# Optimization experiments

Measured on AMD Instinct MI355X. Metric: run time of the kernel, lower is better.

## Reference

```python
import jax, jax.numpy as jnp
import numpy as np

N = 500_000
K = 16
E = N * K
H = 256


def _linear_params(key, fan_in, fan_out):
    k1, k2 = jax.random.split(key)
    bound = 1.0 / np.sqrt(fan_in)
    W = jax.random.uniform(k1, (fan_in, fan_out), jnp.float32, -bound, bound)
    b = jax.random.uniform(k2, (fan_out,), jnp.float32, -bound, bound)
    return W, b


def setup_inputs() -> dict:
    key = jax.random.key(0)
    ks = jax.random.split(key, 10)
    x = jax.random.normal(ks[0], (N, 3), jnp.float32)
    edge_index = jax.random.randint(ks[1], (2, E), 0, N, jnp.int64)
    edge_attr = jax.random.normal(ks[2], (E, 1), jnp.float32)
    W1, b1 = _linear_params(ks[3], K, H)          # GNN1 message MLP: Linear(k, 256)
    We1, be1 = _linear_params(ks[4], H, 128)      # encoder Linear(256,128)
    We2, be2 = _linear_params(ks[5], 128, 6)      # encoder Linear(128,6)
    Wd1, bd1 = _linear_params(ks[6], 6, 128)      # decoder Linear(6,128)
    Wd2, bd2 = _linear_params(ks[7], 128, H)      # decoder Linear(128,256)
    Wo, bo = _linear_params(ks[8], H, 1)          # output Linear(256,1)
    return {"x": x, "edge_index": edge_index, "edge_attr": edge_attr,
            "W1": W1, "b1": b1, "We1": We1, "be1": be1, "We2": We2, "be2": be2,
            "Wd1": Wd1, "bd1": bd1, "Wd2": Wd2, "bd2": bd2, "Wo": Wo, "bo": bo}


def reference(x, edge_index, edge_attr, W1, b1, We1, be1, We2, be2,
              Wd1, bd1, Wd2, bd2, Wo, bo):
    # GNN1: messages are edge_attr verbatim (x_i/x_j ignored); aggregate reshapes
    # all E scalar messages into (N, k) (k edges per node, contiguous) and runs
    # Linear(k,256)+Tanh. Note: LSTM and GCN4 branches in the torch code are dead
    # (GNN1 ignores its node-feature input), so they do not affect the output.
    k = W1.shape[0]
    msgs = edge_attr.reshape(-1, k)                    # (N, k)
    h = jnp.tanh(msgs @ W1 + b1)                       # (N, 256)
    # second L1 call produces the identical result (depends only on edge_attr)
    z = jnp.tanh(jnp.tanh(h @ We1 + be1) @ We2 + be2)  # encoder -> (N, 6)
    d = jnp.tanh(z @ Wd1 + bd1) @ Wd2 + bd2            # decoder -> (N, 256)
    out = jax.nn.sigmoid(jnp.tanh(d) @ Wo + bo)        # (N, 1)
    return out[:, 0]                                   # squeeze(dim=1) -> (N,)
```

## Files before the change

kernel.cpp:

```cpp
#include <hip/hip_runtime.h>


#define N_NODES 500000

#define OFF_W1 0
#define OFF_W2 8192
#define OFF_W3 73728
#define OFF_W4 77824
#define OFF_W5 86016
#define OFF_WO 151552
#define OFF_B1 152576
#define OFF_B2 153600
#define OFF_B3 154112
#define OFF_B4 154176
#define OFF_B5 154688
#define OFF_EXTRA 155712
#define OFF_ZERO  155728
#define IMG_END   156240
#define IMG_ALLOC 156672

#define K1_B1    77824
#define K1_B2    78848
#define K1_B3    79360
#define K1_Z     79872
#define K1_LDS   80384
#define K2_LDS   76800
#define K2_W4    0
#define K2_W5    8192
#define K2_WO    73728
#define K2_B4    74752
#define K2_B5    75264

#define SCONST (-2.8853900817779268f)

typedef _Float16 half8  __attribute__((ext_vector_type(8)));
typedef __fp16   pk16x2 __attribute__((ext_vector_type(2)));
typedef float    f32x4  __attribute__((ext_vector_type(4)));
typedef int      int4v  __attribute__((ext_vector_type(4)));

__device__ __align__(16) char g_img[IMG_ALLOC];

static __device__ __forceinline__ unsigned pack_f16_rne(float a, float b) {
  _Float16 ha = (_Float16)a, hb = (_Float16)b;
  unsigned short ua = __builtin_bit_cast(unsigned short, ha);
  unsigned short ub = __builtin_bit_cast(unsigned short, hb);
  return (unsigned)ua | ((unsigned)ub << 16);
}
static __device__ __forceinline__ int pkrtz(float a, float b) {
  pk16x2 h = __builtin_amdgcn_cvt_pkrtz(a, b);
  return __builtin_bit_cast(int, h);
}
static __device__ __forceinline__ float sig2(float y) {
  float e = __builtin_amdgcn_exp2f(y);
  return __builtin_amdgcn_rcpf(1.0f + e);
}
static __device__ __forceinline__ float sigmoid_f(float x) {
  float e = __builtin_amdgcn_exp2f(x * -1.4426950408889634f);
  return __builtin_amdgcn_rcpf(1.0f + e);
}
static __device__ __forceinline__ f32x4 mfma16(half8 a, int4v b, f32x4 c) {
  return __builtin_amdgcn_mfma_f32_16x16x32_f16(a, __builtin_bit_cast(half8, b), c, 0, 0, 0);
}
static __device__ __forceinline__ half8 lda(const char* smem, int off) {
  return *(const half8*)(smem + off);
}
static __device__ __forceinline__ f32x4 ldf4(const char* smem, int off) {
  return *(const f32x4*)(smem + off);
}
#define FENCE() __builtin_amdgcn_sched_barrier(0)

struct PK2 { int lo, hi; };
static __device__ __forceinline__ PK2 tp(f32x4 a) {
  PK2 p;
  p.lo = pkrtz(sig2(a.x), sig2(a.y));
  p.hi = pkrtz(sig2(a.z), sig2(a.w));
  return p;
}

__global__ void gnn_prep(const float* __restrict__ W1,  const float* __restrict__ b1,
                         const float* __restrict__ We1, const float* __restrict__ be1,
                         const float* __restrict__ We2, const float* __restrict__ be2,
                         const float* __restrict__ Wd1, const float* __restrict__ bd1,
                         const float* __restrict__ Wd2, const float* __restrict__ bd2,
                         const float* __restrict__ Wo,  const float* __restrict__ bo)
{
  int t = blockIdx.x * 256 + threadIdx.x;
  int off = t * 4;
  if (off >= IMG_END) return;
  unsigned val;
  if (off < OFF_W2) {
    int rel = off;
    int mi = rel >> 9, li = (rel >> 4) & 31, j2 = (rel >> 2) & 3;
    int fout = mi * 16 + (li & 15);
    int k0 = (li >> 4) * 8 + j2 * 2;
    val = pack_f16_rne(SCONST * W1[k0 * 256 + fout], SCONST * W1[(k0 + 1) * 256 + fout]);
  } else if (off < OFF_W3) {
    int rel = off - OFF_W2;
    int blk = rel >> 10, li = (rel >> 4) & 63, j2 = (rel >> 2) & 3;
    int mi = blk >> 3, ki = blk & 7;
    int fout = mi * 16 + (li & 15);
    int k0 = ki * 32 + 4 * (li >> 4) + 16 * (j2 >> 1) + 2 * (j2 & 1);
    val = pack_f16_rne(2.0f * SCONST * We1[k0 * 128 + fout],
                       2.0f * SCONST * We1[(k0 + 1) * 128 + fout]);
  } else if (off < OFF_W4) {
    int rel = off - OFF_W3;
    int ki = rel >> 10, li = (rel >> 4) & 63, j2 = (rel >> 2) & 3;
    int fo = li & 15;
    int k0 = ki * 32 + 4 * (li >> 4) + 16 * (j2 >> 1) + 2 * (j2 & 1);
    float a = (fo < 6) ? 2.0f * SCONST * We2[k0 * 6 + fo] : 0.0f;
    float b = (fo < 6) ? 2.0f * SCONST * We2[(k0 + 1) * 6 + fo] : 0.0f;
    val = pack_f16_rne(a, b);
  } else if (off < OFF_W5) {
    int rel = off - OFF_W4;
    int mi = rel >> 10, li = (rel >> 4) & 63, j2 = (rel >> 2) & 3;
    int fout = mi * 16 + (li & 15);
    int qa = li >> 4;
    unsigned v = 0;
    if (j2 < 2) {
      int k0 = 4 * qa + 2 * j2;
      float a = (k0 < 6)     ? 2.0f * SCONST * Wd1[k0 * 128 + fout]       : 0.0f;
      float b = (k0 + 1 < 6) ? 2.0f * SCONST * Wd1[(k0 + 1) * 128 + fout] : 0.0f;
      v = pack_f16_rne(a, b);
    }
    val = v;
  } else if (off < OFF_WO) {
    int rel = off - OFF_W5;
    int blk = rel >> 10, li = (rel >> 4) & 63, j2 = (rel >> 2) & 3;
    int mi = blk >> 2, ki = blk & 3;
    int fout = mi * 16 + (li & 15);
    int k0 = ki * 32 + 4 * (li >> 4) + 16 * (j2 >> 1) + 2 * (j2 & 1);
    val = pack_f16_rne(2.0f * SCONST * Wd2[k0 * 256 + fout],
                       2.0f * SCONST * Wd2[(k0 + 1) * 256 + fout]);
  } else if (off < OFF_B1) {
    val = __builtin_bit_cast(unsigned, 2.0f * Wo[(off - OFF_WO) >> 2]);
  } else if (off < OFF_B2) {
    val = __builtin_bit_cast(unsigned, SCONST * b1[(off - OFF_B1) >> 2]);
  } else if (off < OFF_B3) {
    int i = (off - OFF_B2) >> 2;
    float s = 0.0f;
    for (int k = 0; k < 256; ++k) s += We1[k * 128 + i];
    val = __builtin_bit_cast(unsigned, SCONST * (be1[i] - s));
  } else if (off < OFF_B4) {
    int i = (off - OFF_B3) >> 2;
    float v = 0.0f;
    if (i < 6) {
      float s = 0.0f;
      for (int k = 0; k < 128; ++k) s += We2[k * 6 + i];
      v = SCONST * (be2[i] - s);
    }
    val = __builtin_bit_cast(unsigned, v);
  } else if (off < OFF_B5) {
    int i = (off - OFF_B4) >> 2;
    float s = 0.0f;
    for (int k = 0; k < 6; ++k) s += Wd1[k * 128 + i];
    val = __builtin_bit_cast(unsigned, SCONST * (bd1[i] - s));
  } else if (off < OFF_EXTRA) {
    int i = (off - OFF_B5) >> 2;
    float s = 0.0f;
    for (int k = 0; k < 128; ++k) s += Wd2[k * 256 + i];
    val = __builtin_bit_cast(unsigned, SCONST * (bd2[i] - s));
  } else if (off == OFF_EXTRA) {
    float s = 0.0f;
    for (int k = 0; k < 256; ++k) s += Wo[k];
    val = __builtin_bit_cast(unsigned, bo[0] - s);
  } else {
    val = 0;
  }
  *(unsigned*)(g_img + off) = val;
}

static __device__ __forceinline__ void stage_chunk(const char* src, char* dst) {
  __builtin_amdgcn_global_load_lds(
      (const __attribute__((address_space(1))) void*)src,
      (__attribute__((address_space(3))) void*)dst, 16, 0, 0);
}

#define L1_PAIR(KO, OUT_G0, OUT_G1) do {                                   \
    half8 Ae = lda(smem, w1b + (2*(KO))*w1s);                              \
    half8 Ao = lda(smem, w1b + (2*(KO)+1)*w1s);                            \
    f32x4 be_ = ldf4(smem, K1_B1 + (2*(KO))*64 + q*16);                    \
    f32x4 bo_ = ldf4(smem, K1_B1 + (2*(KO)+1)*64 + q*16);                  \
    f32x4 ae0 = mfma16(Ae, b1g0, be_);                                     \
    f32x4 ae1 = mfma16(Ae, b1g1, be_);                                     \
    f32x4 ao0 = mfma16(Ao, b1g0, bo_);                                     \
    f32x4 ao1 = mfma16(Ao, b1g1, bo_);                                     \
    PK2 pe0 = tp(ae0), po0 = tp(ao0), pe1 = tp(ae1), po1 = tp(ao1);        \
    OUT_G0.x = pe0.lo; OUT_G0.y = pe0.hi; OUT_G0.z = po0.lo; OUT_G0.w = po0.hi; \
    OUT_G1.x = pe1.lo; OUT_G1.y = pe1.hi; OUT_G1.z = po1.lo; OUT_G1.w = po1.hi; \
    FENCE();                                                               \
  } while (0)

#define L2_MI(MI, ACC0, ACC1) do {                                                            \
    f32x4 bb = ldf4(smem, K1_B2 + (MI)*64 + q*16);                                            \
    ACC0 = bb; ACC1 = bb;                                                                     \
    half8 A;                                                                                  \
    A = lda(smem, OFF_W2 + ((MI)*8+0)*1024 + ln*16); ACC0 = mfma16(A, c2g0_0, ACC0); ACC1 = mfma16(A, c2g1_0, ACC1); \
    A = lda(smem, OFF_W2 + ((MI)*8+1)*1024 + ln*16); ACC0 = mfma16(A, c2g0_1, ACC0); ACC1 = mfma16(A, c2g1_1, ACC1); \
    A = lda(smem, OFF_W2 + ((MI)*8+2)*1024 + ln*16); ACC0 = mfma16(A, c2g0_2, ACC0); ACC1 = mfma16(A, c2g1_2, ACC1); \
    A = lda(smem, OFF_W2 + ((MI)*8+3)*1024 + ln*16); ACC0 = mfma16(A, c2g0_3, ACC0); ACC1 = mfma16(A, c2g1_3, ACC1); \
    A = lda(smem, OFF_W2 + ((MI)*8+4)*1024 + ln*16); ACC0 = mfma16(A, c2g0_4, ACC0); ACC1 = mfma16(A, c2g1_4, ACC1); \
    A = lda(smem, OFF_W2 + ((MI)*8+5)*1024 + ln*16); ACC0 = mfma16(A, c2g0_5, ACC0); ACC1 = mfma16(A, c2g1_5, ACC1); \
    A = lda(smem, OFF_W2 + ((MI)*8+6)*1024 + ln*16); ACC0 = mfma16(A, c2g0_6, ACC0); ACC1 = mfma16(A, c2g1_6, ACC1); \
    A = lda(smem, OFF_W2 + ((MI)*8+7)*1024 + ln*16); ACC0 = mfma16(A, c2g0_7, ACC0); ACC1 = mfma16(A, c2g1_7, ACC1); \
  } while (0)

#define L2_PAIR(KO, OUT_G0, OUT_G1) do {                                   \
    f32x4 ve0, ve1, vo0, vo1;                                              \
    L2_MI(2*(KO),   ve0, ve1);                                             \
    FENCE();                                                               \
    L2_MI(2*(KO)+1, vo0, vo1);                                             \
    PK2 pe0 = tp(ve0), po0 = tp(vo0), pe1 = tp(ve1), po1 = tp(vo1);        \
    OUT_G0.x = pe0.lo; OUT_G0.y = pe0.hi; OUT_G0.z = po0.lo; OUT_G0.w = po0.hi; \
    OUT_G1.x = pe1.lo; OUT_G1.y = pe1.hi; OUT_G1.z = po1.lo; OUT_G1.w = po1.hi; \
    FENCE();                                                               \
  } while (0)

__global__ __launch_bounds__(512)
void gnn_k1(const float* __restrict__ ea, int4v* __restrict__ zbuf)
{
  __shared__ __align__(16) char smem[K1_LDS];
  const int tid = threadIdx.x;
  const int wv = tid >> 6, ln = tid & 63;

#pragma unroll 1
  for (int r = 0; r < 10; ++r) {
    int cb = (r * 8 + wv) << 6;
    if (cb < 5024) {
      int src;
      if (cb < 4864)      src = cb * 16;
      else if (cb < 4992) src = OFF_B1 + (cb - 4864) * 16;
      else                src = OFF_ZERO + (cb - 4992) * 16;
      stage_chunk(g_img + src + ln * 16, smem + (size_t)cb * 16 + ln * 16);
    }
  }
  __syncthreads();

  const int q = ln >> 4, c = ln & 15;
  const bool qlo = (q < 2);
  const int lnl16 = (ln & 31) * 16;
  const int w1b = qlo ? (OFF_W1 + lnl16) : (K1_Z + lnl16);
  const int w1s = qlo ? 512 : 0;

  const int NT = (N_NODES + 255) / 256;
#pragma unroll 1
  for (int t = blockIdx.x; t < NT; t += gridDim.x) {
    const int base = t * 256 + wv * 32;

    int nl = base + (q >> 1) * 16 + c;
    if (nl > N_NODES - 1) nl = N_NODES - 1;
    const f32x4* ea4 = (const f32x4*)ea;
    size_t eb = (size_t)nl * 4 + (size_t)((q & 1) * 2);
    f32x4 vlo = ea4[eb];
    f32x4 vhi = ea4[eb + 1];
    int4v b1g0;
    b1g0.x = pkrtz(vlo.x, vlo.y); b1g0.y = pkrtz(vlo.z, vlo.w);
    b1g0.z = pkrtz(vhi.x, vhi.y); b1g0.w = pkrtz(vhi.z, vhi.w);
    int sh = (ln + 32) & 63;
    int4v b1g1;
    b1g1.x = __shfl(b1g0.x, sh, 64); b1g1.y = __shfl(b1g0.y, sh, 64);
    b1g1.z = __shfl(b1g0.z, sh, 64); b1g1.w = __shfl(b1g0.w, sh, 64);

    int4v c2g0_0, c2g0_1, c2g0_2, c2g0_3, c2g0_4, c2g0_5, c2g0_6, c2g0_7;
    int4v c2g1_0, c2g1_1, c2g1_2, c2g1_3, c2g1_4, c2g1_5, c2g1_6, c2g1_7;
    L1_PAIR(0, c2g0_0, c2g1_0);
    L1_PAIR(1, c2g0_1, c2g1_1);
    L1_PAIR(2, c2g0_2, c2g1_2);
    L1_PAIR(3, c2g0_3, c2g1_3);
    L1_PAIR(4, c2g0_4, c2g1_4);
    L1_PAIR(5, c2g0_5, c2g1_5);
    L1_PAIR(6, c2g0_6, c2g1_6);
    L1_PAIR(7, c2g0_7, c2g1_7);

    int4v c3g0_0, c3g0_1, c3g0_2, c3g0_3;
    int4v c3g1_0, c3g1_1, c3g1_2, c3g1_3;
    L2_PAIR(0, c3g0_0, c3g1_0);
    L2_PAIR(1, c3g0_1, c3g1_1);
    L2_PAIR(2, c3g0_2, c3g1_2);
    L2_PAIR(3, c3g0_3, c3g1_3);

    f32x4 bb3 = ldf4(smem, K1_B3 + q * 16);
    f32x4 z0 = bb3, z1 = bb3;
    half8 A;
    A = lda(smem, OFF_W3 + 0 * 1024 + ln * 16); z0 = mfma16(A, c3g0_0, z0); z1 = mfma16(A, c3g1_0, z1);
    A = lda(smem, OFF_W3 + 1 * 1024 + ln * 16); z0 = mfma16(A, c3g0_1, z0); z1 = mfma16(A, c3g1_1, z1);
    A = lda(smem, OFF_W3 + 2 * 1024 + ln * 16); z0 = mfma16(A, c3g0_2, z0); z1 = mfma16(A, c3g1_2, z1);
    A = lda(smem, OFF_W3 + 3 * 1024 + ln * 16); z0 = mfma16(A, c3g0_3, z0); z1 = mfma16(A, c3g1_3, z1);
    PK2 p3g0 = tp(z0);
    PK2 p3g1 = tp(z1);

    if (ln < 32) {
      int4v zv;
      zv.x = p3g0.lo; zv.y = p3g0.hi; zv.z = p3g1.lo; zv.w = p3g1.hi;
      zbuf[(size_t)(t * 8 + wv) * 32 + ln] = zv;
    }
  }
}

#define L4_MI(MI, ACC0, ACC1) do {                                         \
    f32x4 bb = ldf4(smem, K2_B4 + (MI)*64 + q*16);                         \
    half8 A = lda(smem, K2_W4 + (MI)*1024 + ln*16);                        \
    ACC0 = mfma16(A, b4g0, bb);                                            \
    ACC1 = mfma16(A, b4g1, bb);                                            \
  } while (0)

#define L4_PAIR(KO, OUT_G0, OUT_G1) do {                                   \
    f32x4 ve0, ve1, vo0, vo1;                                              \
    L4_MI(2*(KO),   ve0, ve1);                                             \
    L4_MI(2*(KO)+1, vo0, vo1);                                             \
    PK2 pe0 = tp(ve0), po0 = tp(vo0), pe1 = tp(ve1), po1 = tp(vo1);        \
    OUT_G0.x = pe0.lo; OUT_G0.y = pe0.hi; OUT_G0.z = po0.lo; OUT_G0.w = po0.hi; \
    OUT_G1.x = pe1.lo; OUT_G1.y = pe1.hi; OUT_G1.z = po1.lo; OUT_G1.w = po1.hi; \
    FENCE();                                                               \
  } while (0)

#define L5_MI(MI) do {                                                                        \
    f32x4 bb = ldf4(smem, K2_B5 + (MI)*64 + q*16);                                            \
    f32x4 a0 = bb, a1 = bb;                                                                   \
    half8 A;                                                                                  \
    A = lda(smem, K2_W5 + ((MI)*4+0)*1024 + ln*16); a0 = mfma16(A, c5g0_0, a0); a1 = mfma16(A, c5g1_0, a1); \
    A = lda(smem, K2_W5 + ((MI)*4+1)*1024 + ln*16); a0 = mfma16(A, c5g0_1, a0); a1 = mfma16(A, c5g1_1, a1); \
    A = lda(smem, K2_W5 + ((MI)*4+2)*1024 + ln*16); a0 = mfma16(A, c5g0_2, a0); a1 = mfma16(A, c5g1_2, a1); \
    A = lda(smem, K2_W5 + ((MI)*4+3)*1024 + ln*16); a0 = mfma16(A, c5g0_3, a0); a1 = mfma16(A, c5g1_3, a1); \
    f32x4 wo = ldf4(smem, K2_WO + (MI)*64 + q*16);                                            \
    part0 += sig2(a0.x)*wo.x + sig2(a0.y)*wo.y + sig2(a0.z)*wo.z + sig2(a0.w)*wo.w;           \
    part1 += sig2(a1.x)*wo.x + sig2(a1.y)*wo.y + sig2(a1.z)*wo.z + sig2(a1.w)*wo.w;           \
    FENCE();                                                                                  \
  } while (0)

__global__ __launch_bounds__(512)
void gnn_k2(const int4v* __restrict__ zbuf, float* __restrict__ out)
{
  __shared__ __align__(16) char smem[K2_LDS];
  const int tid = threadIdx.x;
  const int wv = tid >> 6, ln = tid & 63;

#pragma unroll 1
  for (int r = 0; r < 10; ++r) {
    int cb = (r * 8 + wv) << 6;
    if (cb < 4800) {
      int src;
      if (cb < 512)       src = OFF_W4 + cb * 16;
      else if (cb < 4672) src = OFF_W5 + (cb - 512) * 16;
      else                src = OFF_B4 + (cb - 4672) * 16;
      stage_chunk(g_img + src + ln * 16, smem + (size_t)cb * 16 + ln * 16);
    }
  }
  __syncthreads();

  const int q = ln >> 4, c = ln & 15;
  const float bo2 = *(const float*)(g_img + OFF_EXTRA);

  const int NT = (N_NODES + 255) / 256;
#pragma unroll 1
  for (int t = blockIdx.x; t < NT; t += gridDim.x) {
    const int base = t * 256 + wv * 32;

    int4v zv = {0, 0, 0, 0};
    if (ln < 32) zv = zbuf[(size_t)(t * 8 + wv) * 32 + ln];

    int4v b4g0, b4g1;
    b4g0.x = zv.x; b4g0.y = zv.y; b4g0.z = 0; b4g0.w = 0;
    b4g1.x = zv.z; b4g1.y = zv.w; b4g1.z = 0; b4g1.w = 0;

    int4v c5g0_0, c5g0_1, c5g0_2, c5g0_3;
    int4v c5g1_0, c5g1_1, c5g1_2, c5g1_3;
    L4_PAIR(0, c5g0_0, c5g1_0);
    L4_PAIR(1, c5g0_1, c5g1_1);
    L4_PAIR(2, c5g0_2, c5g1_2);
    L4_PAIR(3, c5g0_3, c5g1_3);

    float part0 = 0.0f, part1 = 0.0f;
    L5_MI(0);  L5_MI(1);  L5_MI(2);  L5_MI(3);
    L5_MI(4);  L5_MI(5);  L5_MI(6);  L5_MI(7);
    L5_MI(8);  L5_MI(9);  L5_MI(10); L5_MI(11);
    L5_MI(12); L5_MI(13); L5_MI(14); L5_MI(15);

    part0 += __shfl_xor(part0, 16, 64); part0 += __shfl_xor(part0, 32, 64);
    part1 += __shfl_xor(part1, 16, 64); part1 += __shfl_xor(part1, 32, 64);
    if (q < 2) {
      int node = base + q * 16 + c;
      if (node < N_NODES) {
        float v = ((q == 0) ? part0 : part1) + bo2;
        out[node] = sigmoid_f(v);
      }
    }
  }
}

extern "C" void kernel_launch(void* const* d_in, const int* in_sizes, int n_in,
                              void* d_out, int out_size, void* d_ws, size_t ws_size,
                              hipStream_t stream) {
  (void)in_sizes; (void)n_in; (void)ws_size; (void)out_size;
  const float* ea  = (const float*)d_in[2];
  const float* W1  = (const float*)d_in[3];
  const float* b1  = (const float*)d_in[4];
  const float* We1 = (const float*)d_in[5];
  const float* be1 = (const float*)d_in[6];
  const float* We2 = (const float*)d_in[7];
  const float* be2 = (const float*)d_in[8];
  const float* Wd1 = (const float*)d_in[9];
  const float* bd1 = (const float*)d_in[10];
  const float* Wd2 = (const float*)d_in[11];
  const float* bd2 = (const float*)d_in[12];
  const float* Wo  = (const float*)d_in[13];
  const float* bo  = (const float*)d_in[14];

  gnn_prep<<<dim3((IMG_END / 4 + 255) / 256), dim3(256), 0, stream>>>(
      W1, b1, We1, be1, We2, be2, Wd1, bd1, Wd2, bd2, Wo, bo);
  gnn_k1<<<dim3(512), dim3(512), 0, stream>>>(ea, (int4v*)d_ws);
  gnn_k2<<<dim3(512), dim3(512), 0, stream>>>((const int4v*)d_ws, (float*)d_out);
}
```

Measured before the change: 241.2 us.

## Fuse encoder and decoder kernels into one kernel with full weight image in LDS

Merges the two per-node MLP kernels into a single 1024-thread kernel that stages the whole prepared weight image into LDS. The latent vector passes between stages in registers instead of going through a workspace buffer, which removes the global write and read of the intermediate and one kernel launch. The GEMM accumulation chains in the 128-, 6- and 256-wide layers are split into two independent accumulators that are summed at the end, to shorten MFMA dependency chains. The trade-offs are higher per-block LDS use (one block per CU), larger blocks, and register pressure under the new launch bounds, which could cause spills.

New measurement: 292.1 us. 1.21x slower.

```diff
diff --git a/kernel.cpp b/kernel.cpp
--- a/kernel.cpp
+++ b/kernel.cpp
@@ -18,18 +18,7 @@
 #define OFF_ZERO  155728
 #define IMG_END   156240
 #define IMG_ALLOC 156672
-
-#define K1_B1    77824
-#define K1_B2    78848
-#define K1_B3    79360
-#define K1_Z     79872
-#define K1_LDS   80384
-#define K2_LDS   76800
-#define K2_W4    0
-#define K2_W5    8192
-#define K2_WO    73728
-#define K2_B4    74752
-#define K2_B5    75264
+#define ALL_LDS   156672
 
 #define SCONST (-2.8853900817779268f)
 
@@ -175,11 +164,12 @@
       (__attribute__((address_space(3))) void*)dst, 16, 0, 0);
 }
 
+
 #define L1_PAIR(KO, OUT_G0, OUT_G1) do {                                   \
     half8 Ae = lda(smem, w1b + (2*(KO))*w1s);                              \
     half8 Ao = lda(smem, w1b + (2*(KO)+1)*w1s);                            \
-    f32x4 be_ = ldf4(smem, K1_B1 + (2*(KO))*64 + q*16);                    \
-    f32x4 bo_ = ldf4(smem, K1_B1 + (2*(KO)+1)*64 + q*16);                  \
+    f32x4 be_ = ldf4(smem, OFF_B1 + (2*(KO))*64 + q*16);                   \
+    f32x4 bo_ = ldf4(smem, OFF_B1 + (2*(KO)+1)*64 + q*16);                 \
     f32x4 ae0 = mfma16(Ae, b1g0, be_);                                     \
     f32x4 ae1 = mfma16(Ae, b1g1, be_);                                     \
     f32x4 ao0 = mfma16(Ao, b1g0, bo_);                                     \
@@ -191,17 +181,18 @@
   } while (0)
 
 #define L2_MI(MI, ACC0, ACC1) do {                                                            \
-    f32x4 bb = ldf4(smem, K1_B2 + (MI)*64 + q*16);                                            \
-    ACC0 = bb; ACC1 = bb;                                                                     \
+    f32x4 bb = ldf4(smem, OFF_B2 + (MI)*64 + q*16);                                           \
+    f32x4 x0a = bb, x0b = zf4, x1a = bb, x1b = zf4;                                           \
     half8 A;                                                                                  \
-    A = lda(smem, OFF_W2 + ((MI)*8+0)*1024 + ln*16); ACC0 = mfma16(A, c2g0_0, ACC0); ACC1 = mfma16(A, c2g1_0, ACC1); \
-    A = lda(smem, OFF_W2 + ((MI)*8+1)*1024 + ln*16); ACC0 = mfma16(A, c2g0_1, ACC0); ACC1 = mfma16(A, c2g1_1, ACC1); \
-    A = lda(smem, OFF_W2 + ((MI)*8+2)*1024 + ln*16); ACC0 = mfma16(A, c2g0_2, ACC0); ACC1 = mfma16(A, c2g1_2, ACC1); \
-    A = lda(smem, OFF_W2 + ((MI)*8+3)*1024 + ln*16); ACC0 = mfma16(A, c2g0_3, ACC0); ACC1 = mfma16(A, c2g1_3, ACC1); \
-    A = lda(smem, OFF_W2 + ((MI)*8+4)*1024 + ln*16); ACC0 = mfma16(A, c2g0_4, ACC0); ACC1 = mfma16(A, c2g1_4, ACC1); \
-    A = lda(smem, OFF_W2 + ((MI)*8+5)*1024 + ln*16); ACC0 = mfma16(A, c2g0_5, ACC0); ACC1 = mfma16(A, c2g1_5, ACC1); \
-    A = lda(smem, OFF_W2 + ((MI)*8+6)*1024 + ln*16); ACC0 = mfma16(A, c2g0_6, ACC0); ACC1 = mfma16(A, c2g1_6, ACC1); \
-    A = lda(smem, OFF_W2 + ((MI)*8+7)*1024 + ln*16); ACC0 = mfma16(A, c2g0_7, ACC0); ACC1 = mfma16(A, c2g1_7, ACC1); \
+    A = lda(smem, OFF_W2 + ((MI)*8+0)*1024 + ln*16); x0a = mfma16(A, c2g0_0, x0a); x1a = mfma16(A, c2g1_0, x1a); \
+    A = lda(smem, OFF_W2 + ((MI)*8+4)*1024 + ln*16); x0b = mfma16(A, c2g0_4, x0b); x1b = mfma16(A, c2g1_4, x1b); \
+    A = lda(smem, OFF_W2 + ((MI)*8+1)*1024 + ln*16); x0a = mfma16(A, c2g0_1, x0a); x1a = mfma16(A, c2g1_1, x1a); \
+    A = lda(smem, OFF_W2 + ((MI)*8+5)*1024 + ln*16); x0b = mfma16(A, c2g0_5, x0b); x1b = mfma16(A, c2g1_5, x1b); \
+    A = lda(smem, OFF_W2 + ((MI)*8+2)*1024 + ln*16); x0a = mfma16(A, c2g0_2, x0a); x1a = mfma16(A, c2g1_2, x1a); \
+    A = lda(smem, OFF_W2 + ((MI)*8+6)*1024 + ln*16); x0b = mfma16(A, c2g0_6, x0b); x1b = mfma16(A, c2g1_6, x1b); \
+    A = lda(smem, OFF_W2 + ((MI)*8+3)*1024 + ln*16); x0a = mfma16(A, c2g0_3, x0a); x1a = mfma16(A, c2g1_3, x1a); \
+    A = lda(smem, OFF_W2 + ((MI)*8+7)*1024 + ln*16); x0b = mfma16(A, c2g0_7, x0b); x1b = mfma16(A, c2g1_7, x1b); \
+    ACC0 = x0a + x0b; ACC1 = x1a + x1b;                                                       \
   } while (0)
 
 #define L2_PAIR(KO, OUT_G0, OUT_G1) do {                                   \
@@ -215,36 +206,66 @@
     FENCE();                                                               \
   } while (0)
 
-__global__ __launch_bounds__(512)
-void gnn_k1(const float* __restrict__ ea, int4v* __restrict__ zbuf)
+#define L4_MI(MI, ACC0, ACC1) do {                                         \
+    f32x4 bb = ldf4(smem, OFF_B4 + (MI)*64 + q*16);                        \
+    half8 A = lda(smem, OFF_W4 + (MI)*1024 + ln*16);                       \
+    ACC0 = mfma16(A, b4g0, bb);                                            \
+    ACC1 = mfma16(A, b4g1, bb);                                            \
+  } while (0)
+
+#define L4_PAIR(KO, OUT_G0, OUT_G1) do {                                   \
+    f32x4 ve0, ve1, vo0, vo1;                                              \
+    L4_MI(2*(KO),   ve0, ve1);                                             \
+    L4_MI(2*(KO)+1, vo0, vo1);                                             \
+    PK2 pe0 = tp(ve0), po0 = tp(vo0), pe1 = tp(ve1), po1 = tp(vo1);        \
+    OUT_G0.x = pe0.lo; OUT_G0.y = pe0.hi; OUT_G0.z = po0.lo; OUT_G0.w = po0.hi; \
+    OUT_G1.x = pe1.lo; OUT_G1.y = pe1.hi; OUT_G1.z = po1.lo; OUT_G1.w = po1.hi; \
+    FENCE();                                                               \
+  } while (0)
+
+#define L5_MI(MI) do {                                                                        \
+    f32x4 bb = ldf4(smem, OFF_B5 + (MI)*64 + q*16);                                           \
+    f32x4 x0a = bb, x0b = zf4, x1a = bb, x1b = zf4;                                           \
+    half8 A;                                                                                  \
+    A = lda(smem, OFF_W5 + ((MI)*4+0)*1024 + ln*16); x0a = mfma16(A, c5g0_0, x0a); x1a = mfma16(A, c5g1_0, x1a); \
+    A = lda(smem, OFF_W5 + ((MI)*4+2)*1024 + ln*16); x0b = mfma16(A, c5g0_2, x0b); x1b = mfma16(A, c5g1_2, x1b); \
+    A = lda(smem, OFF_W5 + ((MI)*4+1)*1024 + ln*16); x0a = mfma16(A, c5g0_1, x0a); x1a = mfma16(A, c5g1_1, x1a); \
+    A = lda(smem, OFF_W5 + ((MI)*4+3)*1024 + ln*16); x0b = mfma16(A, c5g0_3, x0b); x1b = mfma16(A, c5g1_3, x1b); \
+    f32x4 a0 = x0a + x0b, a1 = x1a + x1b;                                                     \
+    f32x4 wo = ldf4(smem, OFF_WO + (MI)*64 + q*16);                                           \
+    part0 += sig2(a0.x)*wo.x + sig2(a0.y)*wo.y + sig2(a0.z)*wo.z + sig2(a0.w)*wo.w;           \
+    part1 += sig2(a1.x)*wo.x + sig2(a1.y)*wo.y + sig2(a1.z)*wo.z + sig2(a1.w)*wo.w;           \
+    FENCE();                                                                                  \
+  } while (0)
+
+__global__ __launch_bounds__(1024, 4)
+void gnn_all(const float* __restrict__ ea, float* __restrict__ out)
 {
-  __shared__ __align__(16) char smem[K1_LDS];
+  __shared__ __align__(16) char smem[ALL_LDS];
   const int tid = threadIdx.x;
   const int wv = tid >> 6, ln = tid & 63;
 
 #pragma unroll 1
   for (int r = 0; r < 10; ++r) {
-    int cb = (r * 8 + wv) << 6;
-    if (cb < 5024) {
-      int src;
-      if (cb < 4864)      src = cb * 16;
-      else if (cb < 4992) src = OFF_B1 + (cb - 4864) * 16;
-      else                src = OFF_ZERO + (cb - 4992) * 16;
-      stage_chunk(g_img + src + ln * 16, smem + (size_t)cb * 16 + ln * 16);
-    }
+    int cb = r * 16 + wv;
+    if (cb < 153)
+      stage_chunk(g_img + (size_t)cb * 1024 + ln * 16,
+                  smem + (size_t)cb * 1024 + ln * 16);
   }
   __syncthreads();
 
   const int q = ln >> 4, c = ln & 15;
   const bool qlo = (q < 2);
   const int lnl16 = (ln & 31) * 16;
-  const int w1b = qlo ? (OFF_W1 + lnl16) : (K1_Z + lnl16);
+  const int w1b = qlo ? (OFF_W1 + lnl16) : (OFF_ZERO + lnl16);
   const int w1s = qlo ? 512 : 0;
-
-  const int NT = (N_NODES + 255) / 256;
+  const float bo2 = *(const float*)(smem + OFF_EXTRA);
+  const f32x4 zf4 = {0.0f, 0.0f, 0.0f, 0.0f};
+
+  const int NT = (N_NODES + 511) / 512;
 #pragma unroll 1
   for (int t = blockIdx.x; t < NT; t += gridDim.x) {
-    const int base = t * 256 + wv * 32;
+    const int base = t * 512 + wv * 32;
 
     int nl = base + (q >> 1) * 16 + c;
     if (nl > N_NODES - 1) nl = N_NODES - 1;
@@ -278,89 +299,22 @@
     L2_PAIR(2, c3g0_2, c3g1_2);
     L2_PAIR(3, c3g0_3, c3g1_3);
 
-    f32x4 bb3 = ldf4(smem, K1_B3 + q * 16);
-    f32x4 z0 = bb3, z1 = bb3;
-    half8 A;
-    A = lda(smem, OFF_W3 + 0 * 1024 + ln * 16); z0 = mfma16(A, c3g0_0, z0); z1 = mfma16(A, c3g1_0, z1);
-    A = lda(smem, OFF_W3 + 1 * 1024 + ln * 16); z0 = mfma16(A, c3g0_1, z0); z1 = mfma16(A, c3g1_1, z1);
-    A = lda(smem, OFF_W3 + 2 * 1024 + ln * 16); z0 = mfma16(A, c3g0_2, z0); z1 = mfma16(A, c3g1_2, z1);
-    A = lda(smem, OFF_W3 + 3 * 1024 + ln * 16); z0 = mfma16(A, c3g0_3, z0); z1 = mfma16(A, c3g1_3, z1);
-    PK2 p3g0 = tp(z0);
-    PK2 p3g1 = tp(z1);
-
-    if (ln < 32) {
-      int4v zv;
-      zv.x = p3g0.lo; zv.y = p3g0.hi; zv.z = p3g1.lo; zv.w = p3g1.hi;
-      zbuf[(size_t)(t * 8 + wv) * 32 + ln] = zv;
+    f32x4 bb3 = ldf4(smem, OFF_B3 + q * 16);
+    f32x4 z0a = bb3, z0b = zf4, z1a = bb3, z1b = zf4;
+    {
+      half8 A;
+      A = lda(smem, OFF_W3 + 0 * 1024 + ln * 16); z0a = mfma16(A, c3g0_0, z0a); z1a = mfma16(A, c3g1_0, z1a);
+      A = lda(smem, OFF_W3 + 2 * 1024 + ln * 16); z0b = mfma16(A, c3g0_2, z0b); z1b = mfma16(A, c3g1_2, z1b);
+      A = lda(smem, OFF_W3 + 1 * 1024 + ln * 16); z0a = mfma16(A, c3g0_1, z0a); z1a = mfma16(A, c3g1_1, z1a);
+      A = lda(smem, OFF_W3 + 3 * 1024 + ln * 16); z0b = mfma16(A, c3g0_3, z0b); z1b = mfma16(A, c3g1_3, z1b);
     }
-  }
-}
-
-#define L4_MI(MI, ACC0, ACC1) do {                                         \
-    f32x4 bb = ldf4(smem, K2_B4 + (MI)*64 + q*16);                         \
-    half8 A = lda(smem, K2_W4 + (MI)*1024 + ln*16);                        \
-    ACC0 = mfma16(A, b4g0, bb);                                            \
-    ACC1 = mfma16(A, b4g1, bb);                                            \
-  } while (0)
-
-#define L4_PAIR(KO, OUT_G0, OUT_G1) do {                                   \
-    f32x4 ve0, ve1, vo0, vo1;                                              \
-    L4_MI(2*(KO),   ve0, ve1);                                             \
-    L4_MI(2*(KO)+1, vo0, vo1);                                             \
-    PK2 pe0 = tp(ve0), po0 = tp(vo0), pe1 = tp(ve1), po1 = tp(vo1);        \
-    OUT_G0.x = pe0.lo; OUT_G0.y = pe0.hi; OUT_G0.z = po0.lo; OUT_G0.w = po0.hi; \
-    OUT_G1.x = pe1.lo; OUT_G1.y = pe1.hi; OUT_G1.z = po1.lo; OUT_G1.w = po1.hi; \
-    FENCE();                                                               \
-  } while (0)
-
-#define L5_MI(MI) do {                                                                        \
-    f32x4 bb = ldf4(smem, K2_B5 + (MI)*64 + q*16);                                            \
-    f32x4 a0 = bb, a1 = bb;                                                                   \
-    half8 A;                                                                                  \
-    A = lda(smem, K2_W5 + ((MI)*4+0)*1024 + ln*16); a0 = mfma16(A, c5g0_0, a0); a1 = mfma16(A, c5g1_0, a1); \
-    A = lda(smem, K2_W5 + ((MI)*4+1)*1024 + ln*16); a0 = mfma16(A, c5g0_1, a0); a1 = mfma16(A, c5g1_1, a1); \
-    A = lda(smem, K2_W5 + ((MI)*4+2)*1024 + ln*16); a0 = mfma16(A, c5g0_2, a0); a1 = mfma16(A, c5g1_2, a1); \
-    A = lda(smem, K2_W5 + ((MI)*4+3)*1024 + ln*16); a0 = mfma16(A, c5g0_3, a0); a1 = mfma16(A, c5g1_3, a1); \
-    f32x4 wo = ldf4(smem, K2_WO + (MI)*64 + q*16);                                            \
-    part0 += sig2(a0.x)*wo.x + sig2(a0.y)*wo.y + sig2(a0.z)*wo.z + sig2(a0.w)*wo.w;           \
-    part1 += sig2(a1.x)*wo.x + sig2(a1.y)*wo.y + sig2(a1.z)*wo.z + sig2(a1.w)*wo.w;           \
-    FENCE();                                                                                  \
-  } while (0)
-
-__global__ __launch_bounds__(512)
-void gnn_k2(const int4v* __restrict__ zbuf, float* __restrict__ out)
-{
-  __shared__ __align__(16) char smem[K2_LDS];
-  const int tid = threadIdx.x;
-  const int wv = tid >> 6, ln = tid & 63;
-
-#pragma unroll 1
-  for (int r = 0; r < 10; ++r) {
-    int cb = (r * 8 + wv) << 6;
-    if (cb < 4800) {
-      int src;
-      if (cb < 512)       src = OFF_W4 + cb * 16;
-      else if (cb < 4672) src = OFF_W5 + (cb - 512) * 16;
-      else                src = OFF_B4 + (cb - 4672) * 16;
-      stage_chunk(g_img + src + ln * 16, smem + (size_t)cb * 16 + ln * 16);
-    }
-  }
-  __syncthreads();
-
-  const int q = ln >> 4, c = ln & 15;
-  const float bo2 = *(const float*)(g_img + OFF_EXTRA);
-
-  const int NT = (N_NODES + 255) / 256;
-#pragma unroll 1
-  for (int t = blockIdx.x; t < NT; t += gridDim.x) {
-    const int base = t * 256 + wv * 32;
-
-    int4v zv = {0, 0, 0, 0};
-    if (ln < 32) zv = zbuf[(size_t)(t * 8 + wv) * 32 + ln];
+    PK2 p3g0 = tp(z0a + z0b);
+    PK2 p3g1 = tp(z1a + z1b);
+    FENCE();
 
     int4v b4g0, b4g1;
-    b4g0.x = zv.x; b4g0.y = zv.y; b4g0.z = 0; b4g0.w = 0;
-    b4g1.x = zv.z; b4g1.y = zv.w; b4g1.z = 0; b4g1.w = 0;
+    b4g0.x = p3g0.lo; b4g0.y = p3g0.hi; b4g0.z = 0; b4g0.w = 0;
+    b4g1.x = p3g1.lo; b4g1.y = p3g1.hi; b4g1.z = 0; b4g1.w = 0;
 
     int4v c5g0_0, c5g0_1, c5g0_2, c5g0_3;
     int4v c5g1_0, c5g1_1, c5g1_2, c5g1_3;
@@ -390,7 +344,7 @@
 extern "C" void kernel_launch(void* const* d_in, const int* in_sizes, int n_in,
                               void* d_out, int out_size, void* d_ws, size_t ws_size,
                               hipStream_t stream) {
-  (void)in_sizes; (void)n_in; (void)ws_size; (void)out_size;
+  (void)in_sizes; (void)n_in; (void)d_ws; (void)ws_size; (void)out_size;
   const float* ea  = (const float*)d_in[2];
   const float* W1  = (const float*)d_in[3];
   const float* b1  = (const float*)d_in[4];
@@ -407,6 +361,5 @@
 
   gnn_prep<<<dim3((IMG_END / 4 + 255) / 256), dim3(256), 0, stream>>>(
       W1, b1, We1, be1, We2, be2, Wd1, bd1, Wd2, bd2, Wo, bo);
-  gnn_k1<<<dim3(512), dim3(512), 0, stream>>>(ea, (int4v*)d_ws);
-  gnn_k2<<<dim3(512), dim3(512), 0, stream>>>((const int4v*)d_ws, (float*)d_out);
-}
+  gnn_all<<<dim3(256), dim3(1024), 0, stream>>>(ea, (float*)d_out);
+}
```

## Prefetch next tile inputs, split MFMA accumulator chains, fold decoder bias into weights

Applied to the files above, without the earlier changes.

Both kernels now load the next grid-stride tile's inputs (edge attributes in k1, latent z in k2) before computing the current tile, so global-load latency overlaps with MFMA work. The dependent MFMA accumulation chains in L2, L3 and L5 are split into two independent accumulators that are summed at the end, which shortens the dependency chain. The decoder layer-1 bias is folded into the weight image as an extra K column, paired with a constant 1.0 written into the padded z slot. This removes the bias loads in L4. Fences are coarsened to every two L1 pairs. The trade-offs are more live registers and some rounding differences from storing the bias term in fp16.

Result: no change. 243.3 us (+0.9%).

```diff
diff --git a/kernel.cpp b/kernel.cpp
--- a/kernel.cpp
+++ b/kernel.cpp
@@ -118,8 +118,16 @@
     unsigned v = 0;
     if (j2 < 2) {
       int k0 = 4 * qa + 2 * j2;
-      float a = (k0 < 6)     ? 2.0f * SCONST * Wd1[k0 * 128 + fout]       : 0.0f;
-      float b = (k0 + 1 < 6) ? 2.0f * SCONST * Wd1[(k0 + 1) * 128 + fout] : 0.0f;
+      float a, b;
+      if (k0 < 6) {
+        a = 2.0f * SCONST * Wd1[k0 * 128 + fout];
+        b = (k0 + 1 < 6) ? 2.0f * SCONST * Wd1[(k0 + 1) * 128 + fout] : 0.0f;
+      } else if (k0 == 6) {
+        float s = 0.0f;
+        for (int k = 0; k < 6; ++k) s += Wd1[k * 128 + fout];
+        a = SCONST * (bd1[fout] - s);
+        b = 0.0f;
+      } else { a = 0.0f; b = 0.0f; }
       v = pack_f16_rne(a, b);
     }
     val = v;
@@ -187,21 +195,21 @@
     PK2 pe0 = tp(ae0), po0 = tp(ao0), pe1 = tp(ae1), po1 = tp(ao1);        \
     OUT_G0.x = pe0.lo; OUT_G0.y = pe0.hi; OUT_G0.z = po0.lo; OUT_G0.w = po0.hi; \
     OUT_G1.x = pe1.lo; OUT_G1.y = pe1.hi; OUT_G1.z = po1.lo; OUT_G1.w = po1.hi; \
-    FENCE();                                                               \
   } while (0)
 
 #define L2_MI(MI, ACC0, ACC1) do {                                                            \
     f32x4 bb = ldf4(smem, K1_B2 + (MI)*64 + q*16);                                            \
-    ACC0 = bb; ACC1 = bb;                                                                     \
+    f32x4 x0a = bb, x0b = zf4, x1a = bb, x1b = zf4;                                           \
     half8 A;                                                                                  \
-    A = lda(smem, OFF_W2 + ((MI)*8+0)*1024 + ln*16); ACC0 = mfma16(A, c2g0_0, ACC0); ACC1 = mfma16(A, c2g1_0, ACC1); \
-    A = lda(smem, OFF_W2 + ((MI)*8+1)*1024 + ln*16); ACC0 = mfma16(A, c2g0_1, ACC0); ACC1 = mfma16(A, c2g1_1, ACC1); \
-    A = lda(smem, OFF_W2 + ((MI)*8+2)*1024 + ln*16); ACC0 = mfma16(A, c2g0_2, ACC0); ACC1 = mfma16(A, c2g1_2, ACC1); \
-    A = lda(smem, OFF_W2 + ((MI)*8+3)*1024 + ln*16); ACC0 = mfma16(A, c2g0_3, ACC0); ACC1 = mfma16(A, c2g1_3, ACC1); \
-    A = lda(smem, OFF_W2 + ((MI)*8+4)*1024 + ln*16); ACC0 = mfma16(A, c2g0_4, ACC0); ACC1 = mfma16(A, c2g1_4, ACC1); \
-    A = lda(smem, OFF_W2 + ((MI)*8+5)*1024 + ln*16); ACC0 = mfma16(A, c2g0_5, ACC0); ACC1 = mfma16(A, c2g1_5, ACC1); \
-    A = lda(smem, OFF_W2 + ((MI)*8+6)*1024 + ln*16); ACC0 = mfma16(A, c2g0_6, ACC0); ACC1 = mfma16(A, c2g1_6, ACC1); \
-    A = lda(smem, OFF_W2 + ((MI)*8+7)*1024 + ln*16); ACC0 = mfma16(A, c2g0_7, ACC0); ACC1 = mfma16(A, c2g1_7, ACC1); \
+    A = lda(smem, OFF_W2 + ((MI)*8+0)*1024 + ln*16); x0a = mfma16(A, c2g0_0, x0a); x1a = mfma16(A, c2g1_0, x1a); \
+    A = lda(smem, OFF_W2 + ((MI)*8+4)*1024 + ln*16); x0b = mfma16(A, c2g0_4, x0b); x1b = mfma16(A, c2g1_4, x1b); \
+    A = lda(smem, OFF_W2 + ((MI)*8+1)*1024 + ln*16); x0a = mfma16(A, c2g0_1, x0a); x1a = mfma16(A, c2g1_1, x1a); \
+    A = lda(smem, OFF_W2 + ((MI)*8+5)*1024 + ln*16); x0b = mfma16(A, c2g0_5, x0b); x1b = mfma16(A, c2g1_5, x1b); \
+    A = lda(smem, OFF_W2 + ((MI)*8+2)*1024 + ln*16); x0a = mfma16(A, c2g0_2, x0a); x1a = mfma16(A, c2g1_2, x1a); \
+    A = lda(smem, OFF_W2 + ((MI)*8+6)*1024 + ln*16); x0b = mfma16(A, c2g0_6, x0b); x1b = mfma16(A, c2g1_6, x1b); \
+    A = lda(smem, OFF_W2 + ((MI)*8+3)*1024 + ln*16); x0a = mfma16(A, c2g0_3, x0a); x1a = mfma16(A, c2g1_3, x1a); \
+    A = lda(smem, OFF_W2 + ((MI)*8+7)*1024 + ln*16); x0b = mfma16(A, c2g0_7, x0b); x1b = mfma16(A, c2g1_7, x1b); \
+    ACC0 = x0a + x0b; ACC1 = x1a + x1b;                                                       \
   } while (0)
 
 #define L2_PAIR(KO, OUT_G0, OUT_G1) do {                                   \
@@ -240,18 +248,24 @@
   const int lnl16 = (ln & 31) * 16;
   const int w1b = qlo ? (OFF_W1 + lnl16) : (K1_Z + lnl16);
   const int w1s = qlo ? 512 : 0;
-
+  const int4v zi4 = {0, 0, 0, 0};
+  const half8 h8z = __builtin_bit_cast(half8, zi4);
+  (void)h8z;
+  const f32x4 zf4 = {0.0f, 0.0f, 0.0f, 0.0f};
+
+  const f32x4* ea4 = (const f32x4*)ea;
   const int NT = (N_NODES + 255) / 256;
+
+  int nl0 = blockIdx.x * 256 + wv * 32 + (q >> 1) * 16 + c;
+  if (nl0 > N_NODES - 1) nl0 = N_NODES - 1;
+  size_t eb0 = (size_t)nl0 * 4 + (size_t)((q & 1) * 2);
+  f32x4 vlo = ea4[eb0];
+  f32x4 vhi = ea4[eb0 + 1];
+
 #pragma unroll 1
   for (int t = blockIdx.x; t < NT; t += gridDim.x) {
     const int base = t * 256 + wv * 32;
 
-    int nl = base + (q >> 1) * 16 + c;
-    if (nl > N_NODES - 1) nl = N_NODES - 1;
-    const f32x4* ea4 = (const f32x4*)ea;
-    size_t eb = (size_t)nl * 4 + (size_t)((q & 1) * 2);
-    f32x4 vlo = ea4[eb];
-    f32x4 vhi = ea4[eb + 1];
     int4v b1g0;
     b1g0.x = pkrtz(vlo.x, vlo.y); b1g0.y = pkrtz(vlo.z, vlo.w);
     b1g0.z = pkrtz(vhi.x, vhi.y); b1g0.w = pkrtz(vhi.z, vhi.w);
@@ -260,16 +274,26 @@
     b1g1.x = __shfl(b1g0.x, sh, 64); b1g1.y = __shfl(b1g0.y, sh, 64);
     b1g1.z = __shfl(b1g0.z, sh, 64); b1g1.w = __shfl(b1g0.w, sh, 64);
 
+    int nl2 = (t + gridDim.x) * 256 + wv * 32 + (q >> 1) * 16 + c;
+    if (nl2 > N_NODES - 1) nl2 = N_NODES - 1;
+    size_t eb2 = (size_t)nl2 * 4 + (size_t)((q & 1) * 2);
+    f32x4 nlo = ea4[eb2];
+    f32x4 nhi = ea4[eb2 + 1];
+
     int4v c2g0_0, c2g0_1, c2g0_2, c2g0_3, c2g0_4, c2g0_5, c2g0_6, c2g0_7;
     int4v c2g1_0, c2g1_1, c2g1_2, c2g1_3, c2g1_4, c2g1_5, c2g1_6, c2g1_7;
     L1_PAIR(0, c2g0_0, c2g1_0);
     L1_PAIR(1, c2g0_1, c2g1_1);
+    FENCE();
     L1_PAIR(2, c2g0_2, c2g1_2);
     L1_PAIR(3, c2g0_3, c2g1_3);
+    FENCE();
     L1_PAIR(4, c2g0_4, c2g1_4);
     L1_PAIR(5, c2g0_5, c2g1_5);
+    FENCE();
     L1_PAIR(6, c2g0_6, c2g1_6);
     L1_PAIR(7, c2g0_7, c2g1_7);
+    FENCE();
 
     int4v c3g0_0, c3g0_1, c3g0_2, c3g0_3;
     int4v c3g1_0, c3g1_1, c3g1_2, c3g1_3;
@@ -279,28 +303,35 @@
     L2_PAIR(3, c3g0_3, c3g1_3);
 
     f32x4 bb3 = ldf4(smem, K1_B3 + q * 16);
-    f32x4 z0 = bb3, z1 = bb3;
-    half8 A;
-    A = lda(smem, OFF_W3 + 0 * 1024 + ln * 16); z0 = mfma16(A, c3g0_0, z0); z1 = mfma16(A, c3g1_0, z1);
-    A = lda(smem, OFF_W3 + 1 * 1024 + ln * 16); z0 = mfma16(A, c3g0_1, z0); z1 = mfma16(A, c3g1_1, z1);
-    A = lda(smem, OFF_W3 + 2 * 1024 + ln * 16); z0 = mfma16(A, c3g0_2, z0); z1 = mfma16(A, c3g1_2, z1);
-    A = lda(smem, OFF_W3 + 3 * 1024 + ln * 16); z0 = mfma16(A, c3g0_3, z0); z1 = mfma16(A, c3g1_3, z1);
-    PK2 p3g0 = tp(z0);
-    PK2 p3g1 = tp(z1);
+    f32x4 z0a = bb3, z0b = zf4, z1a = bb3, z1b = zf4;
+    {
+      half8 A;
+      A = lda(smem, OFF_W3 + 0 * 1024 + ln * 16); z0a = mfma16(A, c3g0_0, z0a); z1a = mfma16(A, c3g1_0, z1a);
+      A = lda(smem, OFF_W3 + 2 * 1024 + ln * 16); z0b = mfma16(A, c3g0_2, z0b); z1b = mfma16(A, c3g1_2, z1b);
+      A = lda(smem, OFF_W3 + 1 * 1024 + ln * 16); z0a = mfma16(A, c3g0_1, z0a); z1a = mfma16(A, c3g1_1, z1a);
+      A = lda(smem, OFF_W3 + 3 * 1024 + ln * 16); z0b = mfma16(A, c3g0_3, z0b); z1b = mfma16(A, c3g1_3, z1b);
+    }
+    PK2 p3g0 = tp(z0a + z0b);
+    PK2 p3g1 = tp(z1a + z1b);
 
     if (ln < 32) {
       int4v zv;
       zv.x = p3g0.lo; zv.y = p3g0.hi; zv.z = p3g1.lo; zv.w = p3g1.hi;
+      if (q == 1) {
+        zv.y = (zv.y & 0xFFFF0000) | 0x3C00;
+        zv.w = (zv.w & 0xFFFF0000) | 0x3C00;
+      }
       zbuf[(size_t)(t * 8 + wv) * 32 + ln] = zv;
     }
+
+    vlo = nlo; vhi = nhi;
   }
 }
 
 #define L4_MI(MI, ACC0, ACC1) do {                                         \
-    f32x4 bb = ldf4(smem, K2_B4 + (MI)*64 + q*16);                         \
     half8 A = lda(smem, K2_W4 + (MI)*1024 + ln*16);                        \
-    ACC0 = mfma16(A, b4g0, bb);                                            \
-    ACC1 = mfma16(A, b4g1, bb);                                            \
+    ACC0 = mfma16(A, b4g0, zf4);                                           \
+    ACC1 = mfma16(A, b4g1, zf4);                                           \
   } while (0)
 
 #define L4_PAIR(KO, OUT_G0, OUT_G1) do {                                   \
@@ -315,12 +346,13 @@
 
 #define L5_MI(MI) do {                                                                        \
     f32x4 bb = ldf4(smem, K2_B5 + (MI)*64 + q*16);                                            \
-    f32x4 a0 = bb, a1 = bb;                                                                   \
+    f32x4 x0a = bb, x0b = zf4, x1a = bb, x1b = zf4;                                           \
     half8 A;                                                                                  \
-    A = lda(smem, K2_W5 + ((MI)*4+0)*1024 + ln*16); a0 = mfma16(A, c5g0_0, a0); a1 = mfma16(A, c5g1_0, a1); \
-    A = lda(smem, K2_W5 + ((MI)*4+1)*1024 + ln*16); a0 = mfma16(A, c5g0_1, a0); a1 = mfma16(A, c5g1_1, a1); \
-    A = lda(smem, K2_W5 + ((MI)*4+2)*1024 + ln*16); a0 = mfma16(A, c5g0_2, a0); a1 = mfma16(A, c5g1_2, a1); \
-    A = lda(smem, K2_W5 + ((MI)*4+3)*1024 + ln*16); a0 = mfma16(A, c5g0_3, a0); a1 = mfma16(A, c5g1_3, a1); \
+    A = lda(smem, K2_W5 + ((MI)*4+0)*1024 + ln*16); x0a = mfma16(A, c5g0_0, x0a); x1a = mfma16(A, c5g1_0, x1a); \
+    A = lda(smem, K2_W5 + ((MI)*4+2)*1024 + ln*16); x0b = mfma16(A, c5g0_2, x0b); x1b = mfma16(A, c5g1_2, x1b); \
+    A = lda(smem, K2_W5 + ((MI)*4+1)*1024 + ln*16); x0a = mfma16(A, c5g0_1, x0a); x1a = mfma16(A, c5g1_1, x1a); \
+    A = lda(smem, K2_W5 + ((MI)*4+3)*1024 + ln*16); x0b = mfma16(A, c5g0_3, x0b); x1b = mfma16(A, c5g1_3, x1b); \
+    f32x4 a0 = x0a + x0b, a1 = x1a + x1b;                                                     \
     f32x4 wo = ldf4(smem, K2_WO + (MI)*64 + q*16);                                            \
     part0 += sig2(a0.x)*wo.x + sig2(a0.y)*wo.y + sig2(a0.z)*wo.z + sig2(a0.w)*wo.w;           \
     part1 += sig2(a1.x)*wo.x + sig2(a1.y)*wo.y + sig2(a1.z)*wo.z + sig2(a1.w)*wo.w;           \
@@ -349,18 +381,27 @@
 
   const int q = ln >> 4, c = ln & 15;
   const float bo2 = *(const float*)(g_img + OFF_EXTRA);
+  const f32x4 zf4 = {0.0f, 0.0f, 0.0f, 0.0f};
 
   const int NT = (N_NODES + 255) / 256;
+
+  int4v zv = {0, 0, 0, 0};
+  if (ln < 32) zv = zbuf[(size_t)(blockIdx.x * 8 + wv) * 32 + ln];
+
 #pragma unroll 1
   for (int t = blockIdx.x; t < NT; t += gridDim.x) {
     const int base = t * 256 + wv * 32;
 
-    int4v zv = {0, 0, 0, 0};
-    if (ln < 32) zv = zbuf[(size_t)(t * 8 + wv) * 32 + ln];
-
     int4v b4g0, b4g1;
     b4g0.x = zv.x; b4g0.y = zv.y; b4g0.z = 0; b4g0.w = 0;
     b4g1.x = zv.z; b4g1.y = zv.w; b4g1.z = 0; b4g1.w = 0;
+
+    int4v zvn = {0, 0, 0, 0};
+    {
+      int t2 = t + gridDim.x;
+      if (t2 >= NT) t2 = t;
+      if (ln < 32) zvn = zbuf[(size_t)(t2 * 8 + wv) * 32 + ln];
+    }
 
     int4v c5g0_0, c5g0_1, c5g0_2, c5g0_3;
     int4v c5g1_0, c5g1_1, c5g1_2, c5g1_3;
@@ -384,6 +425,8 @@
         out[node] = sigmoid_f(v);
       }
     }
+
+    zv = zvn;
   }
 }
 
```
